# Kernel optimization log

Measured on AMD Instinct MI355X. Metric: run time of the kernel, lower is better.

The kernel has to match this reference:

```python
import jax, jax.numpy as jnp
import numpy as np

LOG2 = float(np.log(2.0))

def _ssp(x):
    # shifted softplus: ln(0.5*(exp(x)+1)) = softplus(x) - ln 2
    return jax.nn.softplus(x) - LOG2

def setup_inputs() -> dict:
    key = jax.random.key(0)
    ks = jax.random.split(key, 8)
    B, N, D = 32, 512, 1024
    H = D // 2
    s = lambda fan_in: 1.0 / np.sqrt(fan_in)
    return {
        "representation": jax.random.normal(ks[0], (B, N, D), jnp.float32),
        "R": jax.random.normal(ks[1], (B, N, 3), jnp.float32),
        "atom_mask": jnp.ones((B, N), jnp.float32),
        "W1": jax.random.normal(ks[2], (D, H), jnp.float32) * s(D),
        "b1": jnp.zeros((H,), jnp.float32),
        "W2": jax.random.normal(ks[3], (H, 1), jnp.float32) * s(H),
        "b2": jnp.zeros((1,), jnp.float32),
        "Wc1": jax.random.normal(ks[4], (D, H), jnp.float32) * s(D),
        "bc1": jnp.zeros((H,), jnp.float32),
        "Wc2": jax.random.normal(ks[5], (H, 1), jnp.float32) * s(H),
        "bc2": jnp.zeros((1,), jnp.float32),
    }

def reference(representation, R, atom_mask, W1, b1, W2, b2, Wc1, bc1, Wc2, bc2):
    B, N, _ = representation.shape
    # Atomwise pyramidal MLP: n_in -> n_in//2 (shifted softplus) -> 1
    yi = _ssp(jnp.einsum("bnd,dh->bnh", representation, W1) + b1)
    yi = jnp.einsum("bnh,ho->bno", yi, W2) + b2            # [B,N,1]
    # masked sum pool over atoms (mean=0, stddev=1 so standardize is identity)
    y = jnp.sum(yi * atom_mask[..., None], axis=1)          # [B,1]

    # pairwise distances with safe sqrt (diag is exactly zero)
    diff = R[:, None, :, :] - R[:, :, None, :]              # [B,N,N,3]
    d2 = jnp.sum(diff * diff, axis=-1)                      # [B,N,N]
    dist = jnp.where(d2 > 0, jnp.sqrt(jnp.where(d2 > 0, d2, 1.0)), 0.0)

    eye = jnp.eye(N, dtype=dist.dtype)
    tot_mask = atom_mask[:, None, :] * atom_mask[:, :, None] * (1.0 - eye)
    keep = (tot_mask != 0).astype(dist.dtype)               # [B,N,N]
    dist = dist * keep

    # charge net: Dense(n_in, n_in//2, ssp) -> Dense(n_in//2, 1)
    q = _ssp(jnp.einsum("bnd,dh->bnh", representation, Wc1) + bc1)
    q = jnp.einsum("bnh,ho->bno", q, Wc2) + bc2             # [B,N,1]

    inv2 = (1e-5 + dist) ** -2                              # [B,N,N]
    coulomb = q[:, :, 0][:, None, :] * inv2 * q             # [B,N,N] (q_j * inv * q_i)
    coulomb = coulomb * keep
    e = jnp.sum(coulomb, axis=(1, 2))                       # [B]

    return y + e[:, None]                                   # [B,1]
```

## Files before the change

kernel.cpp:

```cpp
#include <hip/hip_runtime.h>
#include <math.h>


typedef unsigned short u16;
typedef unsigned int u32;
typedef __bf16 bf16x8 __attribute__((ext_vector_type(8)));
typedef float f32x4 __attribute__((ext_vector_type(4)));

#define GK 1024
#define NT 16

#define GLOAD_LDS16(g, l) __builtin_amdgcn_global_load_lds( \
    (const __attribute__((address_space(1))) void*)(g),     \
    (__attribute__((address_space(3))) void*)(l), 16, 0, 0)

__device__ __forceinline__ u16 f2bf(float f) {
    u32 u = __float_as_uint(f);
    return (u16)((u + 0x7FFFu + ((u >> 16) & 1u)) >> 16);
}

__device__ __forceinline__ float ssp_f(float x) {
    return __logf(0.5f * (__expf(x) + 1.0f));
}

__device__ __forceinline__ float ssp_slow(float x) {
    return fmaxf(x, 0.0f) + log1pf(expf(-fabsf(x))) - 0.6931471805599453f;
}


__global__ __launch_bounds__(256) void prep(
    const float* __restrict__ rep, const float* __restrict__ W1,
    const float* __restrict__ Wc1, u16* __restrict__ Abf,
    u16* __restrict__ Bp, float* __restrict__ out)
{
    __shared__ float tile[32][33];
    const int blk = blockIdx.x;
    const int t = threadIdx.x;
    if (blk < 8192) {
        int i = (blk * 256 + t) * 8;
        float4 x = *(const float4*)(rep + i);
        float4 y = *(const float4*)(rep + i + 4);
        union { u16 h[8]; uint4 v; } o;
        o.h[0] = f2bf(x.x); o.h[1] = f2bf(x.y); o.h[2] = f2bf(x.z); o.h[3] = f2bf(x.w);
        o.h[4] = f2bf(y.x); o.h[5] = f2bf(y.y); o.h[6] = f2bf(y.z); o.h[7] = f2bf(y.w);
        *(uint4*)(Abf + i) = o.v;
        if (blk == 0 && t < 32) out[t] = 0.0f;
    } else {
        const int bb = blk - 8192;
        const int k0 = (bb & 31) * 32;
        const int n0 = (bb >> 5) * 32;
        const float* src = (n0 < 512) ? W1 : Wc1;
        const int ns0 = (n0 < 512) ? n0 : n0 - 512;
#pragma unroll
        for (int j = 0; j < 4; j++) {
            int idx = j * 256 + t;
            int kl = idx >> 5, nl = idx & 31;
            tile[kl][nl] = src[(size_t)(k0 + kl) * 512 + ns0 + nl];
        }
        __syncthreads();
#pragma unroll
        for (int j = 0; j < 4; j++) {
            int idx = j * 256 + t;
            int nl = idx >> 5, kl = idx & 31;
            int n = n0 + nl;
            int c16 = n >> 4, lmv = n & 15;
            int kt32 = k0 >> 5, qv = kl >> 3, jv = kl & 7;
            Bp[(size_t)(((c16 * 32 + kt32) * 64) + qv * 16 + lmv) * 8 + jv] =
                f2bf(tile[kl][nl]);
        }
    }
}


__global__ __launch_bounds__(512, 2) void gemm_mfma(
    const u16* __restrict__ A,
    const u16* __restrict__ Bp,
    const float* __restrict__ b1, const float* __restrict__ W2,
    const float* __restrict__ bc1, const float* __restrict__ Wc2,
    float* __restrict__ parts)
{
    __shared__ u16 smem[2][16384];

    const int blk = blockIdx.x;
    const int swz = ((blk & 7) << 5) | (blk >> 3);
    const int bm = swz >> 2;
    const int bn = swz & 3;
    const int tid = threadIdx.x;
    const int w = tid >> 6, lane = tid & 63;
    const int wm = w & 1, wn = w >> 1;
    const int lm = lane & 15, q = lane >> 4;

    f32x4 acc[8][4];
#pragma unroll
    for (int i = 0; i < 8; i++)
#pragma unroll
        for (int j = 0; j < 4; j++)
            acc[i][j] = (f32x4){0.0f, 0.0f, 0.0f, 0.0f};

    int goff[2][2];
#pragma unroll
    for (int h = 0; h < 2; h++)
#pragma unroll
        for (int p2 = 0; p2 < 2; p2++) {
            int ci = h * 1024 + (w * 2 + p2) * 64 + lane;
            int row = ci >> 3;
            int c = (ci & 7) ^ (row & 7);
            goff[h][p2] = row * GK + c * 8;
        }

    int arow[4], aswz[2];
#pragma unroll
    for (int mi = 0; mi < 4; mi++) arow[mi] = (wm * 128 + mi * 16 + lm) * 64;
#pragma unroll
    for (int kk = 0; kk < 2; kk++) aswz[kk] = ((kk * 4 + q) ^ (lm & 7)) * 8;

    const u16* Ab = A + (size_t)bm * 256 * GK;
    const u16* Bw = Bp + (size_t)(bn * 16 + wn * 4) * 16384 + lane * 8;

#define STAGE_A(G, H, BUF) do {                                               \
    GLOAD_LDS16((G) + goff[H][0], &smem[BUF][((H) * 1024 + (w * 2 + 0) * 64) * 8]); \
    GLOAD_LDS16((G) + goff[H][1], &smem[BUF][((H) * 1024 + (w * 2 + 1) * 64) * 8]); \
} while (0)

#define LOAD_B(DST, T)                                                        \
    _Pragma("unroll") for (int nj = 0; nj < 4; nj++)                          \
    _Pragma("unroll") for (int kk = 0; kk < 2; kk++)                          \
        DST[nj][kk] = *(const bf16x8*)&Bw[nj * 16384 + ((T) * 2 + kk) * 512];

#define READ_A(BUF, MH)                                                       \
    _Pragma("unroll") for (int mi = 0; mi < 4; mi++)                          \
    _Pragma("unroll") for (int kk = 0; kk < 2; kk++)                          \
        afr[mi][kk] = *(const bf16x8*)&smem[BUF][arow[mi] + (MH) * 4096 + aswz[kk]];

#define MFMA_HALF(MH, BF)                                                     \
    _Pragma("unroll") for (int kk = 0; kk < 2; kk++)                          \
    _Pragma("unroll") for (int mi = 0; mi < 4; mi++)                          \
    _Pragma("unroll") for (int nj = 0; nj < 4; nj++)                          \
        acc[(MH) * 4 + mi][nj] = __builtin_amdgcn_mfma_f32_16x16x32_bf16(     \
            afr[mi][kk], BF[nj][kk], acc[(MH) * 4 + mi][nj], 0, 0, 0);

#define TILE_BODY(CUR, BCUR, BNXT, TN) do {                                   \
    const u16* gA_ = Ab + (TN) * 64;                                          \
    STAGE_A(gA_, 0, (CUR) ^ 1);                                               \
    STAGE_A(gA_, 1, (CUR) ^ 1);                                               \
    LOAD_B(BNXT, TN);                                                         \
    READ_A(CUR, 0);                                                           \
    __builtin_amdgcn_s_setprio(1);                                            \
    MFMA_HALF(0, BCUR);                                                       \
    __builtin_amdgcn_s_setprio(0);                                            \
    READ_A(CUR, 1);                                                           \
    __builtin_amdgcn_s_setprio(1);                                            \
    MFMA_HALF(1, BCUR);                                                       \
    __builtin_amdgcn_s_setprio(0);                                            \
    asm volatile("s_waitcnt vmcnt(0) lgkmcnt(0)" ::: "memory");               \
    __builtin_amdgcn_s_barrier();                                             \
} while (0)

    bf16x8 afr[4][2], bA[4][2], bB[4][2];

    STAGE_A(Ab, 0, 0);
    STAGE_A(Ab, 1, 0);
    LOAD_B(bA, 0);
    asm volatile("s_waitcnt vmcnt(0)" ::: "memory");
    __builtin_amdgcn_s_barrier();

    for (int tt = 0; tt < NT / 2; ++tt) {
        const int t0 = 2 * tt, t1 = 2 * tt + 1;
        TILE_BODY(0, bA, bB, ((t0 + 1) & (NT - 1)));
        TILE_BODY(1, bB, bA, ((t1 + 1) & (NT - 1)));
    }

#undef STAGE_A
#undef LOAD_B
#undef READ_A
#undef MFMA_HALF
#undef TILE_BODY

    __syncthreads();
    float* red = (float*)&smem[0][0];
    const bool is_q = (bn >= 2);
    const float* bb2 = is_q ? bc1 : b1;
    const float* vv = is_q ? Wc2 : W2;
    float bias[4], v[4];
#pragma unroll
    for (int nfr = 0; nfr < 4; nfr++) {
        int c = (bn & 1) * 256 + wn * 64 + nfr * 16 + lm;
        bias[nfr] = bb2[c];
        v[nfr] = vv[c];
    }
#pragma unroll
    for (int mfr = 0; mfr < 8; mfr++) {
#pragma unroll
        for (int r = 0; r < 4; r++) {
            float s = 0.0f;
#pragma unroll
            for (int nfr = 0; nfr < 4; nfr++)
                s += v[nfr] * ssp_f(acc[mfr][nfr][r] + bias[nfr]);
            s += __shfl_xor(s, 1);
            s += __shfl_xor(s, 2);
            s += __shfl_xor(s, 4);
            s += __shfl_xor(s, 8);
            if (lm == 0) red[wn * 256 + wm * 128 + mfr * 16 + q * 4 + r] = s;
        }
    }
    __syncthreads();
    if (tid < 256) {
        float val = red[0 * 256 + tid] + red[1 * 256 + tid] +
                    red[2 * 256 + tid] + red[3 * 256 + tid];
        parts[(size_t)bn * 16384 + bm * 256 + tid] = val;
    }
}


__global__ __launch_bounds__(256) void coulomb_k(
    const float* __restrict__ R, const float* __restrict__ mask,
    const float* __restrict__ parts, const float* __restrict__ b2p,
    const float* __restrict__ bc2p, float* __restrict__ out)
{
    const int N = 512;
    const int b = blockIdx.y;
    const int chunk = blockIdx.x;
    __shared__ float Rx[512], Ry[512], Rz[512], QM[512];
    __shared__ float rbuf[4];
    const int tid = threadIdx.x;
    const float bc2 = bc2p[0];
    const float b2 = b2p[0];

    for (int j = tid; j < N; j += 256) {
        int idx = b * N + j;
        float m = mask[idx];
        const float* rp = R + (size_t)idx * 3;
        Rx[j] = rp[0];
        Ry[j] = rp[1];
        Rz[j] = rp[2];
        float qv = parts[2 * 16384 + idx] + parts[3 * 16384 + idx] + bc2;
        QM[j] = qv * m;
    }
    __syncthreads();

    const int i = chunk * 64 + (tid & 63);
    const int js = (tid >> 6) * 128;
    const float xi = Rx[i], yi = Ry[i], zi = Rz[i], qmi = QM[i];
    float e = 0.0f;
    for (int j = js; j < js + 128; j++) {
        float dx = xi - Rx[j];
        float dy = yi - Ry[j];
        float dz = zi - Rz[j];
        float d2 = dx * dx + dy * dy + dz * dz;
        float t = 1e-5f + sqrtf(d2);
        float term = qmi * QM[j] / (t * t);
        e += (j == i) ? 0.0f : term;
    }
    if (tid < 64) {
        int ii = b * N + chunk * 64 + tid;
        float yv = parts[0 * 16384 + ii] + parts[1 * 16384 + ii] + b2;
        e += yv * mask[ii];
    }
    for (int off = 32; off > 0; off >>= 1) e += __shfl_down(e, off, 64);
    if ((tid & 63) == 0) rbuf[tid >> 6] = e;
    __syncthreads();
    if (tid == 0) atomicAdd(&out[b], rbuf[0] + rbuf[1] + rbuf[2] + rbuf[3]);
}


#define BM 128
#define BN 64
#define BK 16

__global__ __launch_bounds__(256) void mlp_gemm(
    const float* __restrict__ A, const float* __restrict__ W1,
    const float* __restrict__ Wc1, const float* __restrict__ b1,
    const float* __restrict__ bc1, const float* __restrict__ W2,
    const float* __restrict__ Wc2, float* __restrict__ yi_part,
    float* __restrict__ q_part)
{
    const int K = 1024;
    const int bm = blockIdx.x;
    const int bn = blockIdx.y;
    const bool is_q = (bn >= 8);
    const float* __restrict__ W = is_q ? Wc1 : W1;
    const int j0 = (bn & 7) * BN;

    __shared__ float As[BK][BM + 4];
    __shared__ float Bs[BK][BN + 4];
    __shared__ float red[BM];

    const int tid = threadIdx.x;
    const int tx = tid & 15;
    const int ty = tid >> 4;

    float acc[8][4];
#pragma unroll
    for (int r = 0; r < 8; r++)
#pragma unroll
        for (int c = 0; c < 4; c++) acc[r][c] = 0.0f;

    const int a_row = tid >> 2;
    const int a_k4 = (tid & 3) * 4;
    const float* Arow0 = A + (size_t)(bm * BM + a_row) * K;
    const float* Arow1 = Arow0 + (size_t)64 * K;
    const int w_k = tid >> 4;
    const int w_j = (tid & 15) * 4;

    for (int kt = 0; kt < K; kt += BK) {
        float4 av0 = *(const float4*)(Arow0 + kt + a_k4);
        float4 av1 = *(const float4*)(Arow1 + kt + a_k4);
        float4 wv = *(const float4*)(W + (size_t)(kt + w_k) * 512 + j0 + w_j);
        __syncthreads();
        As[a_k4 + 0][a_row] = av0.x;
        As[a_k4 + 1][a_row] = av0.y;
        As[a_k4 + 2][a_row] = av0.z;
        As[a_k4 + 3][a_row] = av0.w;
        As[a_k4 + 0][a_row + 64] = av1.x;
        As[a_k4 + 1][a_row + 64] = av1.y;
        As[a_k4 + 2][a_row + 64] = av1.z;
        As[a_k4 + 3][a_row + 64] = av1.w;
        *(float4*)&Bs[w_k][w_j] = wv;
        __syncthreads();
#pragma unroll
        for (int kk = 0; kk < BK; kk++) {
            float4 a0 = *(const float4*)&As[kk][ty * 8];
            float4 a1 = *(const float4*)&As[kk][ty * 8 + 4];
            float4 bv = *(const float4*)&Bs[kk][tx * 4];
            float ar[8] = {a0.x, a0.y, a0.z, a0.w, a1.x, a1.y, a1.z, a1.w};
            float bc[4] = {bv.x, bv.y, bv.z, bv.w};
#pragma unroll
            for (int r = 0; r < 8; r++)
#pragma unroll
                for (int c = 0; c < 4; c++)
                    acc[r][c] = fmaf(ar[r], bc[c], acc[r][c]);
        }
    }

    const float* bb = is_q ? bc1 : b1;
    const float* vv = is_q ? Wc2 : W2;
    float bias[4], v[4];
#pragma unroll
    for (int c = 0; c < 4; c++) {
        bias[c] = bb[j0 + tx * 4 + c];
        v[c] = vv[j0 + tx * 4 + c];
    }
    if (tid < BM) red[tid] = 0.0f;
    __syncthreads();
#pragma unroll
    for (int r = 0; r < 8; r++) {
        float s = 0.0f;
#pragma unroll
        for (int c = 0; c < 4; c++)
            s += v[c] * ssp_slow(acc[r][c] + bias[c]);
        atomicAdd(&red[ty * 8 + r], s);
    }
    __syncthreads();
    float* target = is_q ? q_part : yi_part;
    if (tid < BM) atomicAdd(&target[(size_t)bm * BM + tid], red[tid]);
}

__global__ __launch_bounds__(256) void coulomb_fb(
    const float* __restrict__ R, const float* __restrict__ mask,
    const float* __restrict__ yi_part, const float* __restrict__ q_part,
    const float* __restrict__ b2p, const float* __restrict__ bc2p,
    float* __restrict__ out)
{
    const int N = 512;
    const int b = blockIdx.y;
    const int chunk = blockIdx.x;
    __shared__ float Rx[512], Ry[512], Rz[512], QM[512];
    __shared__ float rbuf[4];
    const int tid = threadIdx.x;
    const float bc2 = bc2p[0];
    const float b2 = b2p[0];

    for (int j = tid; j < N; j += 256) {
        float m = mask[b * N + j];
        const float* rp = R + ((size_t)b * N + j) * 3;
        Rx[j] = rp[0];
        Ry[j] = rp[1];
        Rz[j] = rp[2];
        QM[j] = (q_part[b * N + j] + bc2) * m;
    }
    __syncthreads();

    const int i = chunk * 64 + (tid & 63);
    const int js = (tid >> 6) * 128;
    const float xi = Rx[i], yi = Ry[i], zi = Rz[i], qmi = QM[i];
    float e = 0.0f;
    for (int j = js; j < js + 128; j++) {
        float dx = xi - Rx[j];
        float dy = yi - Ry[j];
        float dz = zi - Rz[j];
        float d2 = dx * dx + dy * dy + dz * dz;
        float t = 1e-5f + sqrtf(d2);
        float term = qmi * QM[j] / (t * t);
        e += (j == i) ? 0.0f : term;
    }
    if (tid < 64) {
        int ii = chunk * 64 + tid;
        e += (yi_part[b * N + ii] + b2) * mask[b * N + ii];
    }
    for (int off = 32; off > 0; off >>= 1) e += __shfl_down(e, off, 64);
    if ((tid & 63) == 0) rbuf[tid >> 6] = e;
    __syncthreads();
    if (tid == 0) atomicAdd(&out[b], rbuf[0] + rbuf[1] + rbuf[2] + rbuf[3]);
}


extern "C" void kernel_launch(void* const* d_in, const int* in_sizes, int n_in,
                              void* d_out, int out_size, void* d_ws, size_t ws_size,
                              hipStream_t stream) {
    const float* rep  = (const float*)d_in[0];
    const float* R    = (const float*)d_in[1];
    const float* mask = (const float*)d_in[2];
    const float* W1   = (const float*)d_in[3];
    const float* b1   = (const float*)d_in[4];
    const float* W2   = (const float*)d_in[5];
    const float* b2   = (const float*)d_in[6];
    const float* Wc1  = (const float*)d_in[7];
    const float* bc1  = (const float*)d_in[8];
    const float* Wc2  = (const float*)d_in[9];
    const float* bc2  = (const float*)d_in[10];
    float* out = (float*)d_out;

    const size_t szA = 16384ull * 1024 * 2;
    const size_t szB = 1024ull * 1024 * 2;
    const size_t szP = 8ull * 16384 * 4;
    const size_t need = szA + szB + szP;

    if (ws_size >= need) {
        u16* Abf = (u16*)d_ws;
        u16* Bpk = (u16*)((char*)d_ws + szA);
        float* parts = (float*)((char*)d_ws + szA + szB);

        prep<<<8192 + 1024, 256, 0, stream>>>(rep, W1, Wc1, Abf, Bpk, out);
        gemm_mfma<<<256, 512, 0, stream>>>(Abf, Bpk, b1, W2, bc1, Wc2, parts);
        coulomb_k<<<dim3(8, 32), 256, 0, stream>>>(R, mask, parts, b2, bc2, out);
    } else {
        float* yi_part = (float*)d_ws;
        float* q_part = yi_part + 16384;
        hipMemsetAsync(d_ws, 0, 2 * 16384 * sizeof(float), stream);
        hipMemsetAsync(d_out, 0, 32 * sizeof(float), stream);
        mlp_gemm<<<dim3(128, 16), 256, 0, stream>>>(rep, W1, Wc1, b1, bc1, W2, Wc2,
                                                    yi_part, q_part);
        coulomb_fb<<<dim3(8, 32), 256, 0, stream>>>(R, mask, yi_part, q_part, b2, bc2, out);
    }
}
```

Baseline: 169.3 us.

## Triple-buffer A tiles in LDS with prefetch distance two and partial waitcnt

Moves the A-operand staging from double to triple buffering in LDS. The next-next tile is issued via global_load_lds while the current one is consumed, and the per-tile wait drops from vmcnt(0) to vmcnt(8), so the newest loads stay in flight across the barrier. The tile loop is fully unrolled with explicit buffer rotation. LDS per block grows from 64KB to 96KB, which may cut occupancy below the 2 blocks per CU that the launch bounds assume. The vmcnt counting has to match the actual load ordering exactly for the results to stay correct.

```diff
diff --git a/kernel.cpp b/kernel.cpp
--- a/kernel.cpp
+++ b/kernel.cpp
@@ -79,7 +79,7 @@
     const float* __restrict__ bc1, const float* __restrict__ Wc2,
     float* __restrict__ parts)
 {
-    __shared__ u16 smem[2][16384];
+    __shared__ u16 smem[3][16384];
 
     const int blk = blockIdx.x;
     const int swz = ((blk & 7) << 5) | (blk >> 3);
@@ -117,9 +117,12 @@
     const u16* Ab = A + (size_t)bm * 256 * GK;
     const u16* Bw = Bp + (size_t)(bn * 16 + wn * 4) * 16384 + lane * 8;
 
-#define STAGE_A(G, H, BUF) do {                                               \
-    GLOAD_LDS16((G) + goff[H][0], &smem[BUF][((H) * 1024 + (w * 2 + 0) * 64) * 8]); \
-    GLOAD_LDS16((G) + goff[H][1], &smem[BUF][((H) * 1024 + (w * 2 + 1) * 64) * 8]); \
+#define STAGE_A3(BUF, TN) do {                                                \
+    const u16* gA_ = Ab + (TN) * 64;                                          \
+    GLOAD_LDS16(gA_ + goff[0][0], &smem[BUF][((w * 2 + 0) * 64) * 8]);        \
+    GLOAD_LDS16(gA_ + goff[0][1], &smem[BUF][((w * 2 + 1) * 64) * 8]);        \
+    GLOAD_LDS16(gA_ + goff[1][0], &smem[BUF][(1024 + (w * 2 + 0) * 64) * 8]); \
+    GLOAD_LDS16(gA_ + goff[1][1], &smem[BUF][(1024 + (w * 2 + 1) * 64) * 8]); \
 } while (0)
 
 #define LOAD_B(DST, T)                                                        \
@@ -139,42 +142,53 @@
         acc[(MH) * 4 + mi][nj] = __builtin_amdgcn_mfma_f32_16x16x32_bf16(     \
             afr[mi][kk], BF[nj][kk], acc[(MH) * 4 + mi][nj], 0, 0, 0);
 
-#define TILE_BODY(CUR, BCUR, BNXT, TN) do {                                   \
-    const u16* gA_ = Ab + (TN) * 64;                                          \
-    STAGE_A(gA_, 0, (CUR) ^ 1);                                               \
-    STAGE_A(gA_, 1, (CUR) ^ 1);                                               \
-    LOAD_B(BNXT, TN);                                                         \
-    READ_A(CUR, 0);                                                           \
+#define TILE(CUR3, NXT3, BCUR, BNXT, TNB, TNA) do {                           \
+    LOAD_B(BNXT, TNB);                                                        \
+    STAGE_A3(NXT3, TNA);                                                      \
+    READ_A(CUR3, 0);                                                          \
     __builtin_amdgcn_s_setprio(1);                                            \
     MFMA_HALF(0, BCUR);                                                       \
     __builtin_amdgcn_s_setprio(0);                                            \
-    READ_A(CUR, 1);                                                           \
+    READ_A(CUR3, 1);                                                          \
     __builtin_amdgcn_s_setprio(1);                                            \
     MFMA_HALF(1, BCUR);                                                       \
     __builtin_amdgcn_s_setprio(0);                                            \
-    asm volatile("s_waitcnt vmcnt(0) lgkmcnt(0)" ::: "memory");               \
+    asm volatile("s_waitcnt vmcnt(8)" ::: "memory");                          \
     __builtin_amdgcn_s_barrier();                                             \
 } while (0)
 
     bf16x8 afr[4][2], bA[4][2], bB[4][2];
 
-    STAGE_A(Ab, 0, 0);
-    STAGE_A(Ab, 1, 0);
     LOAD_B(bA, 0);
+    STAGE_A3(0, 0);
+    STAGE_A3(1, 1);
+    asm volatile("s_waitcnt vmcnt(4)" ::: "memory");
+    __builtin_amdgcn_s_barrier();
+
+    TILE(0, 2, bA, bB,  1,  2);
+    TILE(1, 0, bB, bA,  2,  3);
+    TILE(2, 1, bA, bB,  3,  4);
+    TILE(0, 2, bB, bA,  4,  5);
+    TILE(1, 0, bA, bB,  5,  6);
+    TILE(2, 1, bB, bA,  6,  7);
+    TILE(0, 2, bA, bB,  7,  8);
+    TILE(1, 0, bB, bA,  8,  9);
+    TILE(2, 1, bA, bB,  9, 10);
+    TILE(0, 2, bB, bA, 10, 11);
+    TILE(1, 0, bA, bB, 11, 12);
+    TILE(2, 1, bB, bA, 12, 13);
+    TILE(0, 2, bA, bB, 13, 14);
+    TILE(1, 0, bB, bA, 14, 15);
+    TILE(2, 1, bA, bB, 15,  0);
+    TILE(0, 2, bB, bA,  0,  1);
+
     asm volatile("s_waitcnt vmcnt(0)" ::: "memory");
-    __builtin_amdgcn_s_barrier();
-
-    for (int tt = 0; tt < NT / 2; ++tt) {
-        const int t0 = 2 * tt, t1 = 2 * tt + 1;
-        TILE_BODY(0, bA, bB, ((t0 + 1) & (NT - 1)));
-        TILE_BODY(1, bB, bA, ((t1 + 1) & (NT - 1)));
-    }
-
-#undef STAGE_A
+
+#undef STAGE_A3
 #undef LOAD_B
 #undef READ_A
 #undef MFMA_HALF
-#undef TILE_BODY
+#undef TILE
 
     __syncthreads();
     float* red = (float*)&smem[0][0];
```

Result: slower. 184.7 us (+9.1%).

## Triple-buffer A tiles in LDS with prefetch distance two

Applied to the files above, without the earlier changes.

The GEMM main loop moves from double-buffered A staging with a full vmcnt/lgkmcnt drain per tile to a three-slot LDS ring. A tiles are prefetched two iterations ahead, and each iteration ends with only a barrier. The goal is to take the global-to-LDS wait off the critical path. In exchange, shared memory rises to 96 KB per block, which can cut the two-blocks-per-CU occupancy. B fragments are now loaded right before use instead of a tile ahead, and the cross-wave visibility of the async LDS writes relies on implicit waits.

```diff
diff --git a/kernel.cpp b/kernel.cpp
--- a/kernel.cpp
+++ b/kernel.cpp
@@ -79,7 +79,7 @@
     const float* __restrict__ bc1, const float* __restrict__ Wc2,
     float* __restrict__ parts)
 {
-    __shared__ u16 smem[2][16384];
+    __shared__ u16 smem[3][16384];
 
     const int blk = blockIdx.x;
     const int swz = ((blk & 7) << 5) | (blk >> 3);
@@ -117,9 +117,12 @@
     const u16* Ab = A + (size_t)bm * 256 * GK;
     const u16* Bw = Bp + (size_t)(bn * 16 + wn * 4) * 16384 + lane * 8;
 
-#define STAGE_A(G, H, BUF) do {                                               \
-    GLOAD_LDS16((G) + goff[H][0], &smem[BUF][((H) * 1024 + (w * 2 + 0) * 64) * 8]); \
-    GLOAD_LDS16((G) + goff[H][1], &smem[BUF][((H) * 1024 + (w * 2 + 1) * 64) * 8]); \
+#define STAGE_A3(SB, TN) do {                                                 \
+    const u16* gA_ = Ab + (TN) * 64;                                          \
+    GLOAD_LDS16(gA_ + goff[0][0], (SB) + ((w * 2 + 0) * 64) * 8);             \
+    GLOAD_LDS16(gA_ + goff[0][1], (SB) + ((w * 2 + 1) * 64) * 8);             \
+    GLOAD_LDS16(gA_ + goff[1][0], (SB) + (1024 + (w * 2 + 0) * 64) * 8);      \
+    GLOAD_LDS16(gA_ + goff[1][1], (SB) + (1024 + (w * 2 + 1) * 64) * 8);      \
 } while (0)
 
 #define LOAD_B(DST, T)                                                        \
@@ -127,55 +130,53 @@
     _Pragma("unroll") for (int kk = 0; kk < 2; kk++)                          \
         DST[nj][kk] = *(const bf16x8*)&Bw[nj * 16384 + ((T) * 2 + kk) * 512];
 
-#define READ_A(BUF, MH)                                                       \
+#define READ_A(SB, MH, DST)                                                   \
     _Pragma("unroll") for (int mi = 0; mi < 4; mi++)                          \
     _Pragma("unroll") for (int kk = 0; kk < 2; kk++)                          \
-        afr[mi][kk] = *(const bf16x8*)&smem[BUF][arow[mi] + (MH) * 4096 + aswz[kk]];
-
-#define MFMA_HALF(MH, BF)                                                     \
+        DST[mi][kk] = *(const bf16x8*)&(SB)[arow[mi] + (MH) * 4096 + aswz[kk]];
+
+#define MFMA_HALF(MH, AF, BF)                                                 \
     _Pragma("unroll") for (int kk = 0; kk < 2; kk++)                          \
     _Pragma("unroll") for (int mi = 0; mi < 4; mi++)                          \
     _Pragma("unroll") for (int nj = 0; nj < 4; nj++)                          \
         acc[(MH) * 4 + mi][nj] = __builtin_amdgcn_mfma_f32_16x16x32_bf16(     \
-            afr[mi][kk], BF[nj][kk], acc[(MH) * 4 + mi][nj], 0, 0, 0);
-
-#define TILE_BODY(CUR, BCUR, BNXT, TN) do {                                   \
-    const u16* gA_ = Ab + (TN) * 64;                                          \
-    STAGE_A(gA_, 0, (CUR) ^ 1);                                               \
-    STAGE_A(gA_, 1, (CUR) ^ 1);                                               \
-    LOAD_B(BNXT, TN);                                                         \
-    READ_A(CUR, 0);                                                           \
-    __builtin_amdgcn_s_setprio(1);                                            \
-    MFMA_HALF(0, BCUR);                                                       \
-    __builtin_amdgcn_s_setprio(0);                                            \
-    READ_A(CUR, 1);                                                           \
-    __builtin_amdgcn_s_setprio(1);                                            \
-    MFMA_HALF(1, BCUR);                                                       \
-    __builtin_amdgcn_s_setprio(0);                                            \
-    asm volatile("s_waitcnt vmcnt(0) lgkmcnt(0)" ::: "memory");               \
-    __builtin_amdgcn_s_barrier();                                             \
-} while (0)
-
-    bf16x8 afr[4][2], bA[4][2], bB[4][2];
-
-    STAGE_A(Ab, 0, 0);
-    STAGE_A(Ab, 1, 0);
-    LOAD_B(bA, 0);
+            AF[mi][kk], BF[nj][kk], acc[(MH) * 4 + mi][nj], 0, 0, 0);
+
+    bf16x8 afrX[4][2], afrY[4][2], bf[4][2];
+
+    STAGE_A3(&smem[0][0], 0);
+    STAGE_A3(&smem[1][0], 1);
     asm volatile("s_waitcnt vmcnt(0)" ::: "memory");
+    __builtin_amdgcn_sched_barrier(0);
     __builtin_amdgcn_s_barrier();
-
-    for (int tt = 0; tt < NT / 2; ++tt) {
-        const int t0 = 2 * tt, t1 = 2 * tt + 1;
-        TILE_BODY(0, bA, bB, ((t0 + 1) & (NT - 1)));
-        TILE_BODY(1, bB, bA, ((t1 + 1) & (NT - 1)));
-    }
-
-#undef STAGE_A
+    __builtin_amdgcn_sched_barrier(0);
+
+    for (int t = 0; t < NT; ++t) {
+        u16* sC = &smem[t % 3][0];
+        u16* sN = &smem[(t + 2) % 3][0];
+
+        LOAD_B(bf, t);
+        if (t < NT - 2) STAGE_A3(sN, t + 2);
+
+        READ_A(sC, 0, afrX);
+        READ_A(sC, 1, afrY);
+
+        __builtin_amdgcn_s_setprio(1);
+        MFMA_HALF(0, afrX, bf);
+        MFMA_HALF(1, afrY, bf);
+        __builtin_amdgcn_s_setprio(0);
+
+        __builtin_amdgcn_sched_barrier(0);
+        __builtin_amdgcn_s_barrier();
+        __builtin_amdgcn_sched_barrier(0);
+    }
+
+#undef STAGE_A3
 #undef LOAD_B
 #undef READ_A
 #undef MFMA_HALF
-#undef TILE_BODY
-
+
+    asm volatile("s_waitcnt vmcnt(0)" ::: "memory");
     __syncthreads();
     float* red = (float*)&smem[0][0];
     const bool is_q = (bn >= 2);
```

Measured after the change: 171.1 us. Within noise of the previous version (+1.0%).
